# Optimization experiments

Hardware: AMD Instinct MI355X
Metric: run time of the kernel (lower is better)

The kernel has to match this reference:

```python
import jax, jax.numpy as jnp
import numpy as np

DIM = 1024
NUM_HEADS = 16
HEAD_DIM = DIM // NUM_HEADS
EPS = 1e-6


def setup_inputs() -> dict:
    key = jax.random.key(0)
    ks = jax.random.split(key, 9)
    B, S = 4, 4096
    std = 1.0 / np.sqrt(DIM)
    inp = {
        "x": jax.random.normal(ks[0], (B, S, DIM), dtype=jnp.float32),
        "attention_mask": jnp.ones((B, S), dtype=jnp.float32),
        "Wq": jax.random.normal(ks[1], (DIM, DIM), dtype=jnp.float32) * std,
        "bq": jnp.zeros((DIM,), dtype=jnp.float32),
        "Wk": jax.random.normal(ks[2], (DIM, DIM), dtype=jnp.float32) * std,
        "bk": jnp.zeros((DIM,), dtype=jnp.float32),
        "Wv": jax.random.normal(ks[3], (DIM, DIM), dtype=jnp.float32) * std,
        "bv": jnp.zeros((DIM,), dtype=jnp.float32),
        "Wo": jax.random.normal(ks[4], (DIM, DIM), dtype=jnp.float32) * std,
        "bo": jnp.zeros((DIM,), dtype=jnp.float32),
    }
    return inp


def _phi(x):
    # ELU + 1 feature map (positive-valued kernel features)
    return jax.nn.elu(x) + 1.0


def reference(x, attention_mask, Wq, bq, Wk, bk, Wv, bv, Wo, bo):
    B, S, _ = x.shape
    H, D = NUM_HEADS, HEAD_DIM
    q = (x @ Wq.T + bq).reshape(B, S, H, D)
    k = (x @ Wk.T + bk).reshape(B, S, H, D)
    v = (x @ Wv.T + bv).reshape(B, S, H, D)
    q = _phi(q)
    k = _phi(k)
    m = attention_mask[:, :, None, None]
    k = k * m
    v = v * m
    # kv state: [B, H, D, D]
    kv = jnp.einsum("bshd,bshm->bhdm", k, v)
    qkv = jnp.einsum("bshd,bhdm->bshm", q, kv)
    k_sum = k.sum(axis=1)  # [B, H, D]
    normalizer = jnp.einsum("bshd,bhd->bsh", q, k_sum) + EPS
    out = (qkv / normalizer[..., None]).reshape(B, S, DIM)
    return out @ Wo.T + bo
```

## Files before the change

### kernel.cpp

```cpp
#include <hip/hip_runtime.h>

typedef unsigned short u16;
typedef float f32x4 __attribute__((ext_vector_type(4)));
typedef __bf16 bf16x8 __attribute__((ext_vector_type(8)));
typedef unsigned short us8 __attribute__((ext_vector_type(8)));

#define EPS_ 1e-6f

__device__ __forceinline__ u16 f2bf(float f) {
    unsigned u = __float_as_uint(f);
    u += 0x7FFFu + ((u >> 16) & 1u);
    return (u16)(u >> 16);
}
__device__ __forceinline__ float bf2f(u16 h) {
    return __uint_as_float(((unsigned)h) << 16);
}
__device__ __forceinline__ void gload_lds16(const void* g, void* l) {
    __builtin_amdgcn_global_load_lds(
        (const __attribute__((address_space(1))) void*)g,
        (__attribute__((address_space(3))) void*)l, 16, 0, 0);
}

__global__ __launch_bounds__(256) void f32_to_bf16_kernel(
    const float* __restrict__ src, u16* __restrict__ dst, int n4)
{
    int i = blockIdx.x * 256 + threadIdx.x;
    if (i >= n4) return;
    float4 f = ((const float4*)src)[i];
    ushort4 o;
    o.x = f2bf(f.x); o.y = f2bf(f.y); o.z = f2bf(f.z); o.w = f2bf(f.w);
    ((ushort4*)dst)[i] = o;
}


__device__ __forceinline__ void stage_half(
    const u16* __restrict__ src, int K, int kbase, char* slot, int tid)
{
    const int w = tid >> 6, l = tid & 63;
    #pragma unroll
    for (int j = 0; j < 2; ++j) {
        int c16 = j * 512 + w * 64 + l;
        int row = c16 >> 2;
        int sl  = c16 & 3;
        int ksrc = kbase + ((sl ^ ((row >> 1) & 3)) << 3);
        gload_lds16(src + (size_t)row * K + ksrc, slot + j * 8192 + w * 1024);
    }
}

#define BARRIER()  asm volatile("s_barrier" ::: "memory")
#define VMCNT0()   asm volatile("s_waitcnt vmcnt(0)" ::: "memory")

#define MFMA1(M_, N_, AF_, BF_) \
    acc[M_][N_] = __builtin_amdgcn_mfma_f32_16x16x32_bf16(BF_, AF_, acc[M_][N_], 0, 0, 0)

#define QUAD(M0, A0_, A1_, A2_, A3_, B0_, B1_, B2_, B3_) do { \
    MFMA1(M0+0, 0, A0_, B0_); MFMA1(M0+0, 1, A0_, B1_); MFMA1(M0+0, 2, A0_, B2_); MFMA1(M0+0, 3, A0_, B3_); \
    MFMA1(M0+1, 0, A1_, B0_); MFMA1(M0+1, 1, A1_, B1_); MFMA1(M0+1, 2, A1_, B2_); MFMA1(M0+1, 3, A1_, B3_); \
    MFMA1(M0+2, 0, A2_, B0_); MFMA1(M0+2, 1, A2_, B1_); MFMA1(M0+2, 2, A2_, B2_); MFMA1(M0+2, 3, A2_, B3_); \
    MFMA1(M0+3, 0, A3_, B0_); MFMA1(M0+3, 1, A3_, B1_); MFMA1(M0+3, 2, A3_, B2_); MFMA1(M0+3, 3, A3_, B3_); \
} while (0)

#define RD(dst_, base_, off_) dst_ = *(const bf16x8*)((base_) + (off_))

template<int MODE>
__global__ __launch_bounds__(512, 2) void gemm8p(
    const u16* __restrict__ A, const u16* __restrict__ B,
    const float* __restrict__ bias,
    u16* __restrict__ oq, u16* __restrict__ ok, u16* __restrict__ ov,
    float* __restrict__ outf, int M, int N, int K)
{
    extern __shared__ char lds[];
    const int tid  = threadIdx.x;
    const int lane = tid & 63;
    const int wv   = tid >> 6;
    const int wm   = wv >> 2;
    const int wn   = wv & 3;
    const int NT = K >> 6;

    int bx, by;
    {
        const int gx = gridDim.x;
        int wg  = blockIdx.y * gx + blockIdx.x;
        int cpx = (gx * gridDim.y) >> 3;
        int swz = (wg & 7) * cpx + (wg >> 3);
        bx = swz % gx; by = swz / gx;
    }

    const u16* Ab = A + (size_t)by * 256 * K;
    const u16* Bb = B + (size_t)bx * 256 * K;

    const int i  = lane & 15, g = lane >> 4;
    const int fo = ((g ^ ((i >> 1) & 3)) << 4);
    const int aoff = (wm * 128 + i) * 64 + fo;
    const int boff = (wn * 64 + i) * 64 + fo;

    f32x4 acc[8][4];
    #pragma unroll
    for (int m = 0; m < 8; ++m)
        #pragma unroll
        for (int n = 0; n < 4; ++n) {
            acc[m][n][0] = 0.f; acc[m][n][1] = 0.f;
            acc[m][n][2] = 0.f; acc[m][n][3] = 0.f;
        }

    stage_half(Ab, K, 0,  lds + 0,     tid);
    stage_half(Bb, K, 0,  lds + 16384, tid);
    stage_half(Ab, K, 32, lds + 32768, tid);
    stage_half(Bb, K, 32, lds + 49152, tid);

    for (int t = 0; t < NT; ++t) {
        char* cb = lds + ((t & 1) << 16);
        char* nb = lds + (((t + 1) & 1) << 16);
        const int t1 = (t + 1 < NT) ? t + 1 : NT - 1;

        VMCNT0();
        BARRIER();

        stage_half(Ab, K, t1 * 64,      nb + 0,     tid);
        stage_half(Bb, K, t1 * 64,      nb + 16384, tid);
        stage_half(Ab, K, t1 * 64 + 32, nb + 32768, tid);
        stage_half(Bb, K, t1 * 64 + 32, nb + 49152, tid);

        bf16x8 aL0, aL1, aL2, aL3, aH0, aH1, aH2, aH3, b00, b01, b02, b03;
        bf16x8 cL0, cL1, cL2, cL3, cH0, cH1, cH2, cH3, b10, b11, b12, b13;

        RD(aL0, cb, aoff + 0);    RD(aL1, cb, aoff + 1024);
        RD(aL2, cb, aoff + 2048); RD(aL3, cb, aoff + 3072);
        RD(b00, cb + 16384, boff + 0);    RD(b01, cb + 16384, boff + 1024);
        RD(b02, cb + 16384, boff + 2048); RD(b03, cb + 16384, boff + 3072);
        RD(aH0, cb, aoff + 4096); RD(aH1, cb, aoff + 5120);
        RD(aH2, cb, aoff + 6144); RD(aH3, cb, aoff + 7168);

        QUAD(0, aL0, aL1, aL2, aL3, b00, b01, b02, b03);

        RD(cL0, cb + 32768, aoff + 0);    RD(cL1, cb + 32768, aoff + 1024);
        RD(cL2, cb + 32768, aoff + 2048); RD(cL3, cb + 32768, aoff + 3072);
        RD(b10, cb + 49152, boff + 0);    RD(b11, cb + 49152, boff + 1024);
        RD(b12, cb + 49152, boff + 2048); RD(b13, cb + 49152, boff + 3072);

        QUAD(4, aH0, aH1, aH2, aH3, b00, b01, b02, b03);

        RD(cH0, cb + 32768, aoff + 4096); RD(cH1, cb + 32768, aoff + 5120);
        RD(cH2, cb + 32768, aoff + 6144); RD(cH3, cb + 32768, aoff + 7168);

        QUAD(0, cL0, cL1, cL2, cL3, b10, b11, b12, b13);
        QUAD(4, cH0, cH1, cH2, cH3, b10, b11, b12, b13);
    }
    VMCNT0();

    const int rowg0 = by * 256 + wm * 128;
    const int colg0 = bx * 256 + wn * 64;

    if (MODE == 1) {
        const int which = colg0 >> 10;
        u16* dst = (which == 0) ? oq : ((which == 1) ? ok : ov);
        const bool dophi = (which < 2);
        const int cbo = colg0 & 1023;
        float4 bs[4];
        #pragma unroll
        for (int n = 0; n < 4; ++n)
            bs[n] = *(const float4*)(bias + colg0 + n * 16 + g * 4);
        #pragma unroll
        for (int m = 0; m < 8; ++m) {
            int row = rowg0 + m * 16 + i;
            #pragma unroll
            for (int n = 0; n < 4; ++n) {
                float v0 = acc[m][n][0] + bs[n].x;
                float v1 = acc[m][n][1] + bs[n].y;
                float v2 = acc[m][n][2] + bs[n].z;
                float v3 = acc[m][n][3] + bs[n].w;
                if (dophi) {
                    v0 = (v0 > 0.f) ? (v0 + 1.f) : __expf(v0);
                    v1 = (v1 > 0.f) ? (v1 + 1.f) : __expf(v1);
                    v2 = (v2 > 0.f) ? (v2 + 1.f) : __expf(v2);
                    v3 = (v3 > 0.f) ? (v3 + 1.f) : __expf(v3);
                }
                ushort4 o;
                o.x = f2bf(v0); o.y = f2bf(v1); o.z = f2bf(v2); o.w = f2bf(v3);
                *(ushort4*)(dst + (size_t)row * 1024 + cbo + n * 16 + g * 4) = o;
            }
        }
    } else {
        float4 bs[4];
        #pragma unroll
        for (int n = 0; n < 4; ++n)
            bs[n] = *(const float4*)(bias + colg0 + n * 16 + g * 4);
        #pragma unroll
        for (int m = 0; m < 8; ++m) {
            int row = rowg0 + m * 16 + i;
            #pragma unroll
            for (int n = 0; n < 4; ++n) {
                float4 o;
                o.x = acc[m][n][0] + bs[n].x;
                o.y = acc[m][n][1] + bs[n].y;
                o.z = acc[m][n][2] + bs[n].z;
                o.w = acc[m][n][3] + bs[n].w;
                *(float4*)(outf + (size_t)row * N + colg0 + n * 16 + g * 4) = o;
            }
        }
    }
}

__global__ __launch_bounds__(256) void kv_partial(
    const u16* __restrict__ kbf, const u16* __restrict__ vbf,
    const float* __restrict__ mask, float* __restrict__ kvp, float* __restrict__ ksp)
{
    const int bh = blockIdx.x, ch = blockIdx.y;
    const int b = bh >> 4, h = bh & 15;
    const int tid = threadIdx.x;
    __shared__ __align__(16) float ks[32][64];
    __shared__ __align__(16) float vs[32][64];
    const int dg = tid >> 4, mg = tid & 15;
    float acc[4][4] = {};
    float ksa[4] = {};
    const int s0 = ch * 256;
    const int lr = tid >> 3, lc = (tid & 7) * 8;
    for (int sb = 0; sb < 256; sb += 32) {
        {
            size_t grow = (size_t)b * 4096 + (s0 + sb + lr);
            float mm = mask[grow];
            size_t off = (grow << 10) + (h << 6) + lc;
            us8 ku = __builtin_bit_cast(us8, *(const bf16x8*)(kbf + off));
            us8 vu = __builtin_bit_cast(us8, *(const bf16x8*)(vbf + off));
            #pragma unroll
            for (int j = 0; j < 8; ++j) {
                ks[lr][lc + j] = bf2f(ku[j]) * mm;
                vs[lr][lc + j] = bf2f(vu[j]) * mm;
            }
        }
        __syncthreads();
        #pragma unroll
        for (int ss = 0; ss < 32; ++ss) {
            float4 k4 = *(const float4*)&ks[ss][dg << 2];
            float4 v4 = *(const float4*)&vs[ss][mg << 2];
            float ka[4] = {k4.x, k4.y, k4.z, k4.w};
            float va[4] = {v4.x, v4.y, v4.z, v4.w};
            #pragma unroll
            for (int di = 0; di < 4; ++di) {
                ksa[di] += ka[di];
                #pragma unroll
                for (int mi = 0; mi < 4; ++mi) acc[di][mi] += ka[di] * va[mi];
            }
        }
        __syncthreads();
    }
    float* o = kvp + (((size_t)ch * 64 + bh) << 12);
    #pragma unroll
    for (int di = 0; di < 4; ++di)
        #pragma unroll
        for (int mi = 0; mi < 4; ++mi)
            o[(dg * 4 + di) * 64 + (mg * 4 + mi)] = acc[di][mi];
    if (mg == 0) {
        float* os = ksp + (((size_t)ch * 64 + bh) << 6);
        #pragma unroll
        for (int di = 0; di < 4; ++di) os[dg * 4 + di] = ksa[di];
    }
}

__global__ __launch_bounds__(256) void kv_reduce(
    const float* __restrict__ kvp, const float* __restrict__ ksp,
    u16* __restrict__ kvTbf, u16* __restrict__ ksumbf)
{
    const int bh = blockIdx.x, tid = threadIdx.x;
    for (int idx = tid; idx < 4096; idx += 256) {
        float s = 0.f;
        #pragma unroll
        for (int c = 0; c < 16; ++c) s += kvp[(((size_t)c * 64 + bh) << 12) + idx];
        int d = idx >> 6, m = idx & 63;
        kvTbf[((size_t)bh << 12) + (m << 6) + d] = f2bf(s);
    }
    if (tid < 64) {
        float s = 0.f;
        #pragma unroll
        for (int c = 0; c < 16; ++c) s += ksp[(((size_t)c * 64 + bh) << 6) + tid];
        ksumbf[(bh << 6) + tid] = f2bf(s);
    }
}

__global__ __launch_bounds__(256) void attn_kernel(
    const u16* __restrict__ qbf, const u16* __restrict__ kvTbf,
    const u16* __restrict__ ksumbf, u16* __restrict__ attnbf)
{
    const int bh = blockIdx.x;
    const int b = bh >> 4, h = bh & 15;
    const int tid = threadIdx.x, lane = tid & 63, wv = tid >> 6;
    __shared__ __align__(16) u16 kvs[64 * 64];
    __shared__ __align__(16) u16 kss[64];

    {
        const uint4* src = (const uint4*)(kvTbf + ((size_t)bh << 12));
        for (int u = tid; u < 512; u += 256) {
            uint4 d4 = src[u];
            int m = u >> 3, slot = u & 7;
            *(uint4*)((char*)kvs + m * 128 + ((slot ^ (m & 7)) << 4)) = d4;
        }
        if (tid < 32)
            ((unsigned*)kss)[tid] = ((const unsigned*)(ksumbf + ((size_t)bh << 6)))[tid];
    }
    __syncthreads();

    bf16x8 bfr[2][4], bnf[2];
    #pragma unroll
    for (int kk = 0; kk < 2; ++kk) {
        int kslot = kk * 4 + (lane >> 4);
        #pragma unroll
        for (int n = 0; n < 4; ++n) {
            int m = n * 16 + (lane & 15);
            bfr[kk][n] = *(const bf16x8*)((const char*)kvs + m * 128 +
                                          ((kslot ^ (m & 7)) << 4));
        }
        #pragma unroll
        for (int i2 = 0; i2 < 8; ++i2) bnf[kk][i2] = (__bf16)0.0f;
        if ((lane & 15) == 0)
            bnf[kk] = *(const bf16x8*)((const char*)kss + (kslot << 4));
    }

    const int sbase = blockIdx.y * 256 + wv * 16;
    for (int it = 0; it < 4; ++it) {
        const int st = sbase + it * 64;
        f32x4 acc[4], nacc;
        #pragma unroll
        for (int n = 0; n < 4; ++n) {
            acc[n][0] = 0.f; acc[n][1] = 0.f; acc[n][2] = 0.f; acc[n][3] = 0.f;
        }
        nacc[0] = 0.f; nacc[1] = 0.f; nacc[2] = 0.f; nacc[3] = 0.f;
        #pragma unroll
        for (int kk = 0; kk < 2; ++kk) {
            size_t goff = (((size_t)(b * 4096 + st + (lane & 15))) << 10) +
                          (h << 6) + kk * 32 + ((lane >> 4) << 3);
            bf16x8 af = *(const bf16x8*)(qbf + goff);
            #pragma unroll
            for (int n = 0; n < 4; ++n)
                acc[n] = __builtin_amdgcn_mfma_f32_16x16x32_bf16(af, bfr[kk][n], acc[n], 0, 0, 0);
            nacc = __builtin_amdgcn_mfma_f32_16x16x32_bf16(af, bnf[kk], nacc, 0, 0, 0);
        }
        float inv[4];
        #pragma unroll
        for (int j = 0; j < 4; ++j) {
            float nj = __shfl(nacc[j], lane & 48);
            inv[j] = 1.0f / (nj + EPS_);
        }
        #pragma unroll
        for (int n = 0; n < 4; ++n)
            #pragma unroll
            for (int j = 0; j < 4; ++j) {
                int row = st + ((lane >> 4) << 2) + j;
                attnbf[(((size_t)(b * 4096 + row)) << 10) + (h << 6) + n * 16 + (lane & 15)]
                    = f2bf(acc[n][j] * inv[j]);
            }
    }
}

extern "C" void kernel_launch(void* const* d_in, const int* in_sizes, int n_in,
                              void* d_out, int out_size, void* d_ws, size_t ws_size,
                              hipStream_t stream) {
    const float* x    = (const float*)d_in[0];
    const float* mask = (const float*)d_in[1];
    const float* Wq   = (const float*)d_in[2];
    const float* bq   = (const float*)d_in[3];
    const float* Wk   = (const float*)d_in[4];
    const float* bk   = (const float*)d_in[5];
    const float* Wv   = (const float*)d_in[6];
    const float* bv   = (const float*)d_in[7];
    const float* Wo   = (const float*)d_in[8];
    const float* bo   = (const float*)d_in[9];
    float* out = (float*)d_out;

    if (ws_size < 142606336u) return;

    char* ws = (char*)d_ws;
    u16*   xbf    = (u16*)ws;
    u16*   wqkvbf = (u16*)(ws + 33554432);
    float* bcat   = (float*)(ws + 39845888);
    u16*   qbf    = (u16*)(ws + 41943040);
    u16*   kbf    = qbf + 16777216;
    u16*   vbf    = kbf + 16777216;
    u16*   attnbf = kbf;
    float* kvp    = (float*)ws;
    float* ksp    = (float*)(ws + 16777216);
    u16*   kvTbf  = (u16*)(ws + 17039360);
    u16*   ksumbf = (u16*)(ws + 17563648);
    u16*   wobf   = (u16*)(ws + 20971520);

    f32_to_bf16_kernel<<<16384, 256, 0, stream>>>(x,  xbf,  16777216 / 4);
    f32_to_bf16_kernel<<<1024,  256, 0, stream>>>(Wq, wqkvbf,           1048576 / 4);
    f32_to_bf16_kernel<<<1024,  256, 0, stream>>>(Wk, wqkvbf + 1048576, 1048576 / 4);
    f32_to_bf16_kernel<<<1024,  256, 0, stream>>>(Wv, wqkvbf + 2097152, 1048576 / 4);
    hipMemcpyAsync(bcat,        bq, 4096, hipMemcpyDeviceToDevice, stream);
    hipMemcpyAsync(bcat + 1024, bk, 4096, hipMemcpyDeviceToDevice, stream);
    hipMemcpyAsync(bcat + 2048, bv, 4096, hipMemcpyDeviceToDevice, stream);

    gemm8p<1><<<dim3(12, 64), 512, 131072, stream>>>(
        xbf, wqkvbf, bcat, qbf, kbf, vbf, nullptr, 16384, 3072, 1024);

    f32_to_bf16_kernel<<<1024, 256, 0, stream>>>(Wo, wobf, 1048576 / 4);

    kv_partial<<<dim3(64, 16), 256, 0, stream>>>(kbf, vbf, mask, kvp, ksp);
    kv_reduce<<<64, 256, 0, stream>>>(kvp, ksp, kvTbf, ksumbf);

    attn_kernel<<<dim3(64, 16), 256, 0, stream>>>(qbf, kvTbf, ksumbf, attnbf);

    gemm8p<0><<<dim3(4, 64), 512, 131072, stream>>>(
        attnbf, wobf, bo, nullptr, nullptr, nullptr, out, 16384, 1024, 1024);
}
```

Before: 251.0 us.

## Deepen GEMM prefetch pipeline with split-half staging and explicit LDS waits

The GEMM main loop now prefetches the first K-half of tile t+2 into the current buffer once it has been consumed, and the second half of tile t+1 into the other buffer. This relaxes the global-load wait from vmcnt(0) to vmcnt(4) and adds a mid-iteration barrier. LDS reads become inline-asm ds_read_b128 with hand-placed lgkmcnt waits and sched barriers, and the MFMA groups are wrapped in s_setprio. The aim is to overlap global loads and LDS reads with MFMA work. In exchange it adds an extra barrier, and the hand-counted waits are fragile.

```diff
diff --git a/kernel.cpp b/kernel.cpp
--- a/kernel.cpp
+++ b/kernel.cpp
@@ -4,6 +4,7 @@
 typedef float f32x4 __attribute__((ext_vector_type(4)));
 typedef __bf16 bf16x8 __attribute__((ext_vector_type(8)));
 typedef unsigned short us8 __attribute__((ext_vector_type(8)));
+typedef __attribute__((address_space(3))) const char* lds3_t;
 
 #define EPS_ 1e-6f
 
@@ -48,19 +49,28 @@
 }
 
 #define BARRIER()  asm volatile("s_barrier" ::: "memory")
+#define VMCNT4()   asm volatile("s_waitcnt vmcnt(4)" ::: "memory")
 #define VMCNT0()   asm volatile("s_waitcnt vmcnt(0)" ::: "memory")
+
+#define DSR_(dst_, base_, OFFSTR_) \
+    asm volatile("ds_read_b128 %0, %1 offset:" OFFSTR_ \
+                 : "=v"(dst_) : "v"((lds3_t)(base_)))
+#define DSR(dst_, base_, OFF_) DSR_(dst_, base_, #OFF_)
+
+#define LGKM_(NSTR_) asm volatile("s_waitcnt lgkmcnt(" NSTR_ ")" ::: "memory")
+#define LGKM(N_) do { LGKM_(#N_); __builtin_amdgcn_sched_barrier(0); } while (0)
 
 #define MFMA1(M_, N_, AF_, BF_) \
     acc[M_][N_] = __builtin_amdgcn_mfma_f32_16x16x32_bf16(BF_, AF_, acc[M_][N_], 0, 0, 0)
 
 #define QUAD(M0, A0_, A1_, A2_, A3_, B0_, B1_, B2_, B3_) do { \
+    __builtin_amdgcn_s_setprio(1); \
     MFMA1(M0+0, 0, A0_, B0_); MFMA1(M0+0, 1, A0_, B1_); MFMA1(M0+0, 2, A0_, B2_); MFMA1(M0+0, 3, A0_, B3_); \
     MFMA1(M0+1, 0, A1_, B0_); MFMA1(M0+1, 1, A1_, B1_); MFMA1(M0+1, 2, A1_, B2_); MFMA1(M0+1, 3, A1_, B3_); \
     MFMA1(M0+2, 0, A2_, B0_); MFMA1(M0+2, 1, A2_, B1_); MFMA1(M0+2, 2, A2_, B2_); MFMA1(M0+2, 3, A2_, B3_); \
     MFMA1(M0+3, 0, A3_, B0_); MFMA1(M0+3, 1, A3_, B1_); MFMA1(M0+3, 2, A3_, B2_); MFMA1(M0+3, 3, A3_, B3_); \
+    __builtin_amdgcn_s_setprio(0); \
 } while (0)
-
-#define RD(dst_, base_, off_) dst_ = *(const bf16x8*)((base_) + (off_))
 
 template<int MODE>
 __global__ __launch_bounds__(512, 2) void gemm8p(
@@ -103,47 +113,54 @@
             acc[m][n][2] = 0.f; acc[m][n][3] = 0.f;
         }
 
-    stage_half(Ab, K, 0,  lds + 0,     tid);
-    stage_half(Bb, K, 0,  lds + 16384, tid);
-    stage_half(Ab, K, 32, lds + 32768, tid);
-    stage_half(Bb, K, 32, lds + 49152, tid);
+    stage_half(Ab, K, 0,  lds + 0,             tid);
+    stage_half(Bb, K, 0,  lds + 16384,         tid);
+    stage_half(Ab, K, 32, lds + 32768,         tid);
+    stage_half(Bb, K, 32, lds + 49152,         tid);
+    stage_half(Ab, K, 64, lds + 65536 + 0,     tid);
+    stage_half(Bb, K, 64, lds + 65536 + 16384, tid);
 
     for (int t = 0; t < NT; ++t) {
         char* cb = lds + ((t & 1) << 16);
         char* nb = lds + (((t + 1) & 1) << 16);
         const int t1 = (t + 1 < NT) ? t + 1 : NT - 1;
-
-        VMCNT0();
+        const int t2 = (t + 2 < NT) ? t + 2 : NT - 1;
+
+        VMCNT4();
         BARRIER();
 
-        stage_half(Ab, K, t1 * 64,      nb + 0,     tid);
-        stage_half(Bb, K, t1 * 64,      nb + 16384, tid);
+        const char* aK0 = cb + aoff;
+        const char* bK0 = cb + 16384 + boff;
+        const char* aK1 = cb + 32768 + aoff;
+        const char* bK1 = cb + 49152 + boff;
+
+        bf16x8 aL0, aL1, aL2, aL3, aH0, aH1, aH2, aH3, b00, b01, b02, b03;
+        bf16x8 cL0, cL1, cL2, cL3, cH0, cH1, cH2, cH3, b10, b11, b12, b13;
+
+        DSR(b00, bK0, 0); DSR(b01, bK0, 1024); DSR(b02, bK0, 2048); DSR(b03, bK0, 3072);
+        DSR(aL0, aK0, 0); DSR(aL1, aK0, 1024); DSR(aL2, aK0, 2048); DSR(aL3, aK0, 3072);
+        DSR(aH0, aK0, 4096); DSR(aH1, aK0, 5120); DSR(aH2, aK0, 6144); DSR(aH3, aK0, 7168);
+
         stage_half(Ab, K, t1 * 64 + 32, nb + 32768, tid);
         stage_half(Bb, K, t1 * 64 + 32, nb + 49152, tid);
 
-        bf16x8 aL0, aL1, aL2, aL3, aH0, aH1, aH2, aH3, b00, b01, b02, b03;
-        bf16x8 cL0, cL1, cL2, cL3, cH0, cH1, cH2, cH3, b10, b11, b12, b13;
-
-        RD(aL0, cb, aoff + 0);    RD(aL1, cb, aoff + 1024);
-        RD(aL2, cb, aoff + 2048); RD(aL3, cb, aoff + 3072);
-        RD(b00, cb + 16384, boff + 0);    RD(b01, cb + 16384, boff + 1024);
-        RD(b02, cb + 16384, boff + 2048); RD(b03, cb + 16384, boff + 3072);
-        RD(aH0, cb, aoff + 4096); RD(aH1, cb, aoff + 5120);
-        RD(aH2, cb, aoff + 6144); RD(aH3, cb, aoff + 7168);
-
+        LGKM(4);
         QUAD(0, aL0, aL1, aL2, aL3, b00, b01, b02, b03);
 
-        RD(cL0, cb + 32768, aoff + 0);    RD(cL1, cb + 32768, aoff + 1024);
-        RD(cL2, cb + 32768, aoff + 2048); RD(cL3, cb + 32768, aoff + 3072);
-        RD(b10, cb + 49152, boff + 0);    RD(b11, cb + 49152, boff + 1024);
-        RD(b12, cb + 49152, boff + 2048); RD(b13, cb + 49152, boff + 3072);
-
+        DSR(b10, bK1, 0); DSR(b11, bK1, 1024); DSR(b12, bK1, 2048); DSR(b13, bK1, 3072);
+        DSR(cL0, aK1, 0); DSR(cL1, aK1, 1024); DSR(cL2, aK1, 2048); DSR(cL3, aK1, 3072);
+        DSR(cH0, aK1, 4096); DSR(cH1, aK1, 5120); DSR(cH2, aK1, 6144); DSR(cH3, aK1, 7168);
+
+        LGKM(12);
         QUAD(4, aH0, aH1, aH2, aH3, b00, b01, b02, b03);
 
-        RD(cH0, cb + 32768, aoff + 4096); RD(cH1, cb + 32768, aoff + 5120);
-        RD(cH2, cb + 32768, aoff + 6144); RD(cH3, cb + 32768, aoff + 7168);
-
+        BARRIER();
+        stage_half(Ab, K, t2 * 64, cb + 0,     tid);
+        stage_half(Bb, K, t2 * 64, cb + 16384, tid);
+
+        LGKM(4);
         QUAD(0, cL0, cL1, cL2, cL3, b10, b11, b12, b13);
+        LGKM(0);
         QUAD(4, cH0, cH1, cH2, cH3, b10, b11, b12, b13);
     }
     VMCNT0();
```

Result: faster. 233.6 us (-6.9%).
